# Optimization experiments

Hardware: AMD Instinct MI355X
Metric: run time of the kernel (lower is better)

## Reference

```python
import jax, jax.numpy as jnp
import numpy as np

N_NODES = 25000
N_EDGES = 250000
F_IN = 32
F_OUT = 32
EDGE_DIM = 6
H1, H2 = 64, 128


def setup_inputs() -> dict:
    key = jax.random.key(0)
    ks = jax.random.split(key, 10)
    s = 0.05
    return {
        "x": jax.random.normal(ks[0], (N_NODES, F_IN), dtype=jnp.float32),
        "edge_attr": jax.random.normal(ks[1], (N_EDGES, EDGE_DIM), dtype=jnp.float32),
        # fnet MLP params: Linear(6->64), ReLU, Linear(64->128), ReLU, Linear(128->F_IN*F_OUT)
        "W1": jax.random.normal(ks[2], (H1, EDGE_DIM), dtype=jnp.float32) * s,
        "b1": jnp.zeros((H1,), dtype=jnp.float32),
        "W2": jax.random.normal(ks[3], (H2, H1), dtype=jnp.float32) * s,
        "b2": jnp.zeros((H2,), dtype=jnp.float32),
        "W3": jax.random.normal(ks[4], (F_IN * F_OUT, H2), dtype=jnp.float32) * s,
        "b3": jnp.zeros((F_IN * F_OUT,), dtype=jnp.float32),
        "edge_src": jax.random.randint(ks[5], (N_EDGES,), 0, N_NODES),
        "edge_dst": jax.random.randint(ks[6], (N_EDGES,), 0, N_NODES),
    }


def reference(x, edge_attr, W1, b1, W2, b2, W3, b3, edge_src, edge_dst):
    # fnet: per-edge MLP producing a dynamic filter theta_e of shape [F_OUT, F_IN]
    h = jax.nn.relu(edge_attr @ W1.T + b1)            # [E, H1]
    h = jax.nn.relu(h @ W2.T + b2)                    # [E, H2]
    theta = (h @ W3.T + b3).reshape(-1, F_OUT, F_IN)  # [E, F_OUT, F_IN]
    # gather source features, apply per-edge filter
    msg = jnp.einsum('eoi,ei->eo', theta, x[edge_src])  # [E, F_OUT]
    # scatter-mean over destination nodes (ECC averages over neighborhood)
    agg = jax.ops.segment_sum(msg, edge_dst, num_segments=N_NODES)
    deg = jax.ops.segment_sum(jnp.ones((msg.shape[0],), x.dtype), edge_dst,
                              num_segments=N_NODES)
    out = agg / jnp.maximum(deg, 1.0)[:, None]        # [N, F_OUT]
    return jax.nn.relu(out)                           # trailing 'r' in config
```

## Files before the change

### kernel.cpp

```cpp
#include <hip/hip_runtime.h>
#include <hip/hip_fp16.h>

#define N_NODES 25000
#define N_EDGES 250000
#define ED 6
#define H1 64
#define H2 128
#define NBLK 977
#define NCHUNK 33
#define CHUNK_USH 4096
#define W3S_USHORTS (NCHUNK*CHUNK_USH)
#define W2S_USHORTS (H2*H1)
#define SCAN_BLOCKS 98

typedef float f32x4 __attribute__((ext_vector_type(4)));
typedef float f32x16 __attribute__((ext_vector_type(16)));
typedef _Float16 f16x8 __attribute__((ext_vector_type(8)));
typedef __fp16 fp16x2 __attribute__((ext_vector_type(2)));
typedef unsigned int u32x4 __attribute__((ext_vector_type(4)));
typedef unsigned int u32x2 __attribute__((ext_vector_type(2)));

union F16x8U { u32x4 u; f16x8 h; };
union PKU    { fp16x2 p; unsigned u; };

__device__ __forceinline__ unsigned pkrtz(float lo, float hi) {
    PKU r; r.p = __builtin_amdgcn_cvt_pkrtz(lo, hi); return r.u;
}
__device__ __forceinline__ unsigned pk_mul_blo(unsigned h, unsigned x) {
    unsigned d;
    asm("v_pk_mul_f16 %0, %1, %2 op_sel:[0,0] op_sel_hi:[0,1]" : "=v"(d) : "v"(h), "v"(x));
    return d;
}
__device__ __forceinline__ unsigned pk_mul_bhi(unsigned h, unsigned x) {
    unsigned d;
    asm("v_pk_mul_f16 %0, %1, %2 op_sel:[1,0] op_sel_hi:[1,1]" : "=v"(d) : "v"(h), "v"(x));
    return d;
}
__device__ __forceinline__ f32x4 mfma16(f16x8 a, f16x8 b, f32x4 c) {
    return __builtin_amdgcn_mfma_f32_16x16x32_f16(a, b, c, 0, 0, 0);
}
__device__ __forceinline__ f32x16 mfma32(f16x8 a, f16x8 b, f32x16 c) {
    return __builtin_amdgcn_mfma_f32_32x32x16_f16(a, b, c, 0, 0, 0);
}
__device__ __forceinline__ void gload16(const void* g, void* l) {
    __builtin_amdgcn_global_load_lds(
        (const __attribute__((address_space(1))) unsigned int*)g,
        (__attribute__((address_space(3))) unsigned int*)l, 16, 0, 0);
}

__global__ __launch_bounds__(256) void ecc_init(
    const float* __restrict__ W3, const float* __restrict__ b3,
    const float* __restrict__ W2,
    unsigned* __restrict__ cnt, unsigned short* __restrict__ w3s,
    unsigned short* __restrict__ w2s, float* __restrict__ agg)
{
    int idx = blockIdx.x * 256 + threadIdx.x;
    if (idx < W3S_USHORTS) {
        int c = idx >> 12, r = idx & 4095;
        int ks = r >> 9;
        int lane = (r >> 3) & 63;
        int j = r & 7;
        int o = lane & 31;
        int kp = c * 128 + ks * 16 + ((lane >> 5) << 3) + j;
        float v = 0.f;
        if (kp < 4096)      { int k = kp >> 5, i = kp & 31; v = W3[(o * 32 + i) * 128 + k]; }
        else if (kp < 4128) { v = b3[o * 32 + (kp - 4096)]; }
        __half hv = __float2half_rn(v);
        w3s[idx] = *reinterpret_cast<unsigned short*>(&hv);
    }
    if (idx < W2S_USHORTS) {
        __half hv = __float2half_rn(W2[idx]);
        w2s[idx] = *reinterpret_cast<unsigned short*>(&hv);
    }
    if (idx < N_NODES) cnt[idx] = 0u;
    if (idx < N_NODES * 32) agg[idx] = 0.f;
}

__global__ __launch_bounds__(256) void ecc_hist(
    const int* __restrict__ dst, unsigned* __restrict__ cnt,
    unsigned* __restrict__ rank)
{
    int e = blockIdx.x * 256 + threadIdx.x;
    if (e < N_EDGES) rank[e] = atomicAdd(&cnt[dst[e]], 1u);
}

__global__ __launch_bounds__(256) void ecc_scan1(
    const unsigned* __restrict__ cnt, unsigned* __restrict__ off,
    unsigned* __restrict__ bsum)
{
    __shared__ unsigned s[256];
    const int t = threadIdx.x, i = blockIdx.x * 256 + t;
    unsigned v = (i < N_NODES) ? cnt[i] : 0u;
    s[t] = v; __syncthreads();
    #pragma unroll
    for (int d = 1; d < 256; d <<= 1) {
        unsigned add = (t >= d) ? s[t - d] : 0u;
        __syncthreads(); s[t] += add; __syncthreads();
    }
    if (i < N_NODES) off[i] = s[t] - v;
    if (t == 255) bsum[blockIdx.x] = s[255];
}

__global__ __launch_bounds__(256) void ecc_scan23(
    unsigned* __restrict__ off, const unsigned* __restrict__ bsum)
{
    __shared__ unsigned sbase;
    const int t = threadIdx.x, b = blockIdx.x;
    if (t < 64) {
        unsigned v = 0u;
        if (t < b) v = bsum[t];
        if (t + 64 < b) v += bsum[t + 64];
        #pragma unroll
        for (int d = 32; d >= 1; d >>= 1) v += __shfl_down(v, d, 64);
        if (t == 0) sbase = v;
    }
    __syncthreads();
    const int i = b * 256 + t;
    if (i < N_NODES) off[i] += sbase;
    if (b == 0 && t == 0) off[N_NODES] = N_EDGES;
}

__global__ __launch_bounds__(256) void ecc_perm(
    const int* __restrict__ dst, const unsigned* __restrict__ off,
    const unsigned* __restrict__ rank, unsigned* __restrict__ perm,
    int* __restrict__ bfirst)
{
    int e = blockIdx.x * 256 + threadIdx.x;
    if (e < N_EDGES) perm[off[dst[e]] + rank[e]] = (unsigned)e;
    if (e < NBLK) {
        const unsigned tile = (unsigned)e * 256u;
        int loN = 0, hiN = N_NODES;
        while (loN < hiN) {
            int mid = (loN + hiN) >> 1;
            if (off[mid + 1] > tile) hiN = mid; else loN = mid + 1;
        }
        bfirst[e] = loN;
    }
}

__global__ __launch_bounds__(256) void ecc_fused(
    const float* __restrict__ x,   const float* __restrict__ ea,
    const float* __restrict__ W1,  const float* __restrict__ b1,
    const unsigned short* __restrict__ w2s, const float* __restrict__ b2,
    const unsigned short* __restrict__ w3s,
    const int* __restrict__ src,   const unsigned* __restrict__ perm,
    const unsigned* __restrict__ off, const int* __restrict__ bfirst,
    float* __restrict__ agg)
{
    __shared__ __align__(16) unsigned short sm[256 * H2];
    __shared__ __align__(16) unsigned short wbuf[2][CHUNK_USH];

    const int t = threadIdx.x;
    const int tile = blockIdx.x * 256;
    const int slot = tile + t;
    const bool ev = (slot < N_EDGES);
    const unsigned je = ev ? perm[slot] : 0u;

    const int w = t >> 6, l = t & 63, lr = l & 15, kg = l >> 4;
    const int l31 = l & 31, l5 = l >> 5;

    gload16(w3s + t * 8,        &wbuf[0][t * 8]);
    gload16(w3s + 2048 + t * 8, &wbuf[0][2048 + t * 8]);

    {
        float a[ED];
        #pragma unroll
        for (int c = 0; c < ED; ++c) a[c] = ev ? ea[(long)je * ED + c] : 0.f;

        float h1[H1];
        #pragma unroll
        for (int o = 0; o < H1; ++o) {
            float acc = b1[o];
            #pragma unroll
            for (int c = 0; c < ED; ++c) acc = fmaf(W1[o * ED + c], a[c], acc);
            h1[o] = fmaxf(acc, 0.f);
        }
        #pragma unroll
        for (int q = 0; q < 8; ++q) {
            u32x4 pk;
            #pragma unroll
            for (int j = 0; j < 4; ++j)
                pk[j] = pkrtz(h1[q*8 + 2*j], h1[q*8 + 2*j + 1]);
            const int boff = (t * 128 + q * 16) ^ ((t & 7) << 4);
            *(u32x4*)((char*)sm + boff) = pk;
        }
    }

    unsigned xsh[2][8];
    #pragma unroll
    for (int mt = 0; mt < 2; ++mt) {
        const int er = tile + w * 64 + mt * 32 + l31;
        if (er < N_EDGES) {
            const float* xb = x + (long)src[perm[er]] * 32;
            const float4* xp = (const float4*)(xb + l5 * 8);
            const float4* xq = (const float4*)(xb + 16 + l5 * 8);
            float4 v0 = xp[0], v1 = xp[1], v2 = xq[0], v3 = xq[1];
            xsh[mt][0] = pkrtz(v0.x, v0.y); xsh[mt][1] = pkrtz(v0.z, v0.w);
            xsh[mt][2] = pkrtz(v1.x, v1.y); xsh[mt][3] = pkrtz(v1.z, v1.w);
            xsh[mt][4] = pkrtz(v2.x, v2.y); xsh[mt][5] = pkrtz(v2.z, v2.w);
            xsh[mt][6] = pkrtz(v3.x, v3.y); xsh[mt][7] = pkrtz(v3.z, v3.w);
        } else {
            #pragma unroll
            for (int j = 0; j < 8; ++j) xsh[mt][j] = 0u;
        }
    }

    {
        F16x8U hb[4][2];
        #pragma unroll
        for (int ne = 0; ne < 4; ++ne) {
            const int er = w * 64 + ne * 16 + lr;
            #pragma unroll
            for (int ks = 0; ks < 2; ++ks) {
                const int boff = (er * 128 + ks * 64 + kg * 16) ^ ((er & 7) << 4);
                hb[ne][ks].u = *(const u32x4*)((const char*)sm + boff);
            }
        }
        __syncthreads();

        #pragma unroll
        for (int mo = 0; mo < 8; ++mo) {
            F16x8U a2[2];
            #pragma unroll
            for (int ks = 0; ks < 2; ++ks)
                a2[ks].u = *(const u32x4*)(w2s + (mo*16 + lr) * 64 + ks*32 + kg*8);
            const float4 bv = *(const float4*)(b2 + mo*16 + kg*4);
            #pragma unroll
            for (int ne = 0; ne < 4; ++ne) {
                f32x4 c = (f32x4){0.f, 0.f, 0.f, 0.f};
                c = mfma16(a2[0].h, hb[ne][0].h, c);
                c = mfma16(a2[1].h, hb[ne][1].h, c);
                const unsigned p0 = pkrtz(fmaxf(c[0]+bv.x, 0.f), fmaxf(c[1]+bv.y, 0.f));
                const unsigned p1 = pkrtz(fmaxf(c[2]+bv.z, 0.f), fmaxf(c[3]+bv.w, 0.f));
                const int er = w * 64 + ne * 16 + lr;
                const int boff = (er * 256 + (mo*16 + kg*4) * 2) ^ ((er & 7) << 4);
                *(u32x2*)((char*)sm + boff) = (u32x2){p0, p1};
            }
        }
    }

    f32x16 acc[2];
    #pragma unroll
    for (int i = 0; i < 16; ++i) { acc[0][i] = 0.f; acc[1][i] = 0.f; }

    __syncthreads();

    int cur = 0;
    #pragma unroll 1
    for (int c = 0; c < 32; ++c) {
        {
            const unsigned short* gs = w3s + (c + 1) * CHUNK_USH + t * 8;
            gload16(gs,        &wbuf[cur ^ 1][t * 8]);
            gload16(gs + 2048, &wbuf[cur ^ 1][2048 + t * 8]);
        }
        const char* wb = (const char*)wbuf[cur] + l * 16;

        u32x2 hv[2];
        #pragma unroll
        for (int mt = 0; mt < 2; ++mt) {
            const int row = w * 64 + mt * 32 + l31;
            const int boff = (row * 256 + c * 8) ^ ((row & 7) << 4);
            hv[mt] = *(const u32x2*)((const char*)sm + boff);
        }

        #pragma unroll
        for (int ks = 0; ks < 8; ++ks) {
            F16x8U bf;
            bf.u = *(const u32x4*)(wb + ks * 1024);
            const int kl = ks >> 1;
            const int xb = (ks & 1) * 4;
            #pragma unroll
            for (int mt = 0; mt < 2; ++mt) {
                const unsigned h01 = hv[mt][kl >> 1];
                F16x8U af;
                if (kl & 1) {
                    af.u[0] = pk_mul_bhi(h01, xsh[mt][xb + 0]);
                    af.u[1] = pk_mul_bhi(h01, xsh[mt][xb + 1]);
                    af.u[2] = pk_mul_bhi(h01, xsh[mt][xb + 2]);
                    af.u[3] = pk_mul_bhi(h01, xsh[mt][xb + 3]);
                } else {
                    af.u[0] = pk_mul_blo(h01, xsh[mt][xb + 0]);
                    af.u[1] = pk_mul_blo(h01, xsh[mt][xb + 1]);
                    af.u[2] = pk_mul_blo(h01, xsh[mt][xb + 2]);
                    af.u[3] = pk_mul_blo(h01, xsh[mt][xb + 3]);
                }
                acc[mt] = mfma32(af.h, bf.h, acc[mt]);
            }
        }

        __syncthreads();
        cur ^= 1;
    }
    {
        const char* wb = (const char*)wbuf[cur] + l * 16;
        F16x8U bf0, bf1;
        bf0.u = *(const u32x4*)(wb);
        bf1.u = *(const u32x4*)(wb + 1024);
        #pragma unroll
        for (int mt = 0; mt < 2; ++mt) {
            F16x8U af;
            af.u = (u32x4){xsh[mt][0], xsh[mt][1], xsh[mt][2], xsh[mt][3]};
            acc[mt] = mfma32(af.h, bf0.h, acc[mt]);
            af.u = (u32x4){xsh[mt][4], xsh[mt][5], xsh[mt][6], xsh[mt][7]};
            acc[mt] = mfma32(af.h, bf1.h, acc[mt]);
        }
    }

    __syncthreads();
    {
        unsigned short* msgl = (unsigned short*)sm;
        #pragma unroll
        for (int mt = 0; mt < 2; ++mt) {
            #pragma unroll
            for (int rg = 0; rg < 16; ++rg) {
                const int el = w * 64 + mt * 32 + (rg & 3) + 8 * (rg >> 2) + 4 * l5;
                PKU hv2; hv2.p = __builtin_amdgcn_cvt_pkrtz(acc[mt][rg], 0.f);
                msgl[el * 32 + l31] = (unsigned short)(hv2.u & 0xFFFFu);
            }
        }
    }
    __syncthreads();

    {
        const unsigned short* msgl = (const unsigned short*)sm;
        const int n0 = bfirst[blockIdx.x];
        const int tend = tile + 256;
        #pragma unroll 1
        for (int p = t; ; p += 256) {
            const int n = n0 + (p >> 5);
            if (n >= N_NODES) break;
            const unsigned lo = off[n], hi = off[n + 1];
            if ((int)lo >= tend) break;
            const int o = p & 31;
            const int jb = max((int)lo, tile), jend = min((int)hi, tend);
            if (jend > jb) {
                float s = 0.f;
                for (int j = jb; j < jend; ++j) {
                    union { unsigned short u; _Float16 h; } v;
                    v.u = msgl[(j - tile) * 32 + o];
                    s += (float)v.h;
                }
                atomicAdd(&agg[(long)n * 32 + o], s);
            }
        }
    }
}

__global__ __launch_bounds__(256) void ecc_finalize(
    const float* __restrict__ agg, const unsigned* __restrict__ cnt,
    float* __restrict__ out)
{
    const int i = blockIdx.x * 256 + threadIdx.x;
    if (i >= N_NODES * 32) return;
    const int n = i >> 5;
    const float d = fmaxf((float)cnt[n], 1.f);
    out[i] = fmaxf(agg[i] / d, 0.f);
}

extern "C" void kernel_launch(void* const* d_in, const int* in_sizes, int n_in,
                              void* d_out, int out_size, void* d_ws, size_t ws_size,
                              hipStream_t stream) {
    const float* x   = (const float*)d_in[0];
    const float* ea  = (const float*)d_in[1];
    const float* W1  = (const float*)d_in[2];
    const float* b1  = (const float*)d_in[3];
    const float* W2  = (const float*)d_in[4];
    const float* b2  = (const float*)d_in[5];
    const float* W3  = (const float*)d_in[6];
    const float* b3  = (const float*)d_in[7];
    const int*   src = (const int*)d_in[8];
    const int*   dst = (const int*)d_in[9];
    float* out = (float*)d_out;

    char* p = (char*)d_ws;
    unsigned short* w3s = (unsigned short*)p; p += W3S_USHORTS * 2;
    unsigned short* w2s = (unsigned short*)p; p += 16384;
    unsigned* cnt   = (unsigned*)p; p += 100096;
    unsigned* off   = (unsigned*)p; p += 100352;
    unsigned* bsum  = (unsigned*)p; p += 512;
    int*      bfirst= (int*)p;      p += 4096;
    unsigned* rank  = (unsigned*)p; p += 1000192;
    unsigned* perm  = (unsigned*)p; p += 1000192;
    float*    agg   = (float*)p;

    ecc_init<<<(N_NODES * 32 + 255) / 256, 256, 0, stream>>>(W3, b3, W2, cnt, w3s, w2s, agg);
    ecc_hist<<<NBLK, 256, 0, stream>>>(dst, cnt, rank);
    ecc_scan1<<<SCAN_BLOCKS, 256, 0, stream>>>(cnt, off, bsum);
    ecc_scan23<<<SCAN_BLOCKS, 256, 0, stream>>>(off, bsum);
    ecc_perm<<<NBLK, 256, 0, stream>>>(dst, off, rank, perm, bfirst);
    ecc_fused<<<NBLK, 256, 0, stream>>>(x, ea, W1, b1, w2s, b2, w3s, src, perm, off, bfirst, agg);
    ecc_finalize<<<(N_NODES * 32 + 255) / 256, 256, 0, stream>>>(agg, cnt, out);
}
```

Before: 125.0 us.

## Halve edges per block to 128 and split layer-1 work across thread halves

The fused kernel now processes 128 edges per 256-thread block instead of 256, launching twice as many blocks. Each wave handles one 32-row MFMA tile rather than two, and the two thread halves split the 64 hidden units of layer 1. This halves accumulator and register state and shared memory per block, aiming for higher occupancy and better load balance, at the cost of streaming W3 chunks from global memory twice as often per edge. It also raises wave priority around the MFMA loop and stores messages in shared memory as fp32 instead of fp16, which avoids the conversions and keeps full precision before the atomic adds.

```diff
diff --git a/kernel.cpp b/kernel.cpp
--- a/kernel.cpp
+++ b/kernel.cpp
@@ -7,6 +7,8 @@
 #define H1 64
 #define H2 128
 #define NBLK 977
+#define EPB 128
+#define NBLK2 1954
 #define NCHUNK 33
 #define CHUNK_USH 4096
 #define W3S_USHORTS (NCHUNK*CHUNK_USH)
@@ -127,8 +129,8 @@
 {
     int e = blockIdx.x * 256 + threadIdx.x;
     if (e < N_EDGES) perm[off[dst[e]] + rank[e]] = (unsigned)e;
-    if (e < NBLK) {
-        const unsigned tile = (unsigned)e * 256u;
+    if (e < NBLK2) {
+        const unsigned tile = (unsigned)e * EPB;
         int loN = 0, hiN = N_NODES;
         while (loN < hiN) {
             int mid = (loN + hiN) >> 1;
@@ -147,69 +149,72 @@
     const unsigned* __restrict__ off, const int* __restrict__ bfirst,
     float* __restrict__ agg)
 {
-    __shared__ __align__(16) unsigned short sm[256 * H2];
+    __shared__ __align__(16) unsigned short sm[EPB * H2];
     __shared__ __align__(16) unsigned short wbuf[2][CHUNK_USH];
 
     const int t = threadIdx.x;
-    const int tile = blockIdx.x * 256;
-    const int slot = tile + t;
-    const bool ev = (slot < N_EDGES);
-    const unsigned je = ev ? perm[slot] : 0u;
+    const int tile = blockIdx.x * EPB;
 
     const int w = t >> 6, l = t & 63, lr = l & 15, kg = l >> 4;
     const int l31 = l & 31, l5 = l >> 5;
+    const int e_loc = t & 127, half = t >> 7;
 
     gload16(w3s + t * 8,        &wbuf[0][t * 8]);
     gload16(w3s + 2048 + t * 8, &wbuf[0][2048 + t * 8]);
 
     {
+        const int slot = tile + e_loc;
+        const bool ev = (slot < N_EDGES);
+        const unsigned je = ev ? perm[slot] : 0u;
         float a[ED];
         #pragma unroll
         for (int c = 0; c < ED; ++c) a[c] = ev ? ea[(long)je * ED + c] : 0.f;
 
-        float h1[H1];
-        #pragma unroll
-        for (int o = 0; o < H1; ++o) {
+        float h1[32];
+        #pragma unroll
+        for (int o2 = 0; o2 < 32; ++o2) {
+            const int o = half * 32 + o2;
             float acc = b1[o];
             #pragma unroll
             for (int c = 0; c < ED; ++c) acc = fmaf(W1[o * ED + c], a[c], acc);
-            h1[o] = fmaxf(acc, 0.f);
-        }
-        #pragma unroll
-        for (int q = 0; q < 8; ++q) {
+            h1[o2] = fmaxf(acc, 0.f);
+        }
+        #pragma unroll
+        for (int q = 0; q < 4; ++q) {
             u32x4 pk;
             #pragma unroll
             for (int j = 0; j < 4; ++j)
                 pk[j] = pkrtz(h1[q*8 + 2*j], h1[q*8 + 2*j + 1]);
-            const int boff = (t * 128 + q * 16) ^ ((t & 7) << 4);
+            const int boff = (e_loc * 128 + half * 64 + q * 16) ^ ((e_loc & 7) << 4);
             *(u32x4*)((char*)sm + boff) = pk;
         }
     }
 
-    unsigned xsh[2][8];
-    #pragma unroll
-    for (int mt = 0; mt < 2; ++mt) {
-        const int er = tile + w * 64 + mt * 32 + l31;
+    __syncthreads();
+
+    unsigned xsh[8];
+    {
+        const int er = tile + w * 32 + l31;
         if (er < N_EDGES) {
             const float* xb = x + (long)src[perm[er]] * 32;
             const float4* xp = (const float4*)(xb + l5 * 8);
             const float4* xq = (const float4*)(xb + 16 + l5 * 8);
             float4 v0 = xp[0], v1 = xp[1], v2 = xq[0], v3 = xq[1];
-            xsh[mt][0] = pkrtz(v0.x, v0.y); xsh[mt][1] = pkrtz(v0.z, v0.w);
-            xsh[mt][2] = pkrtz(v1.x, v1.y); xsh[mt][3] = pkrtz(v1.z, v1.w);
-            xsh[mt][4] = pkrtz(v2.x, v2.y); xsh[mt][5] = pkrtz(v2.z, v2.w);
-            xsh[mt][6] = pkrtz(v3.x, v3.y); xsh[mt][7] = pkrtz(v3.z, v3.w);
+            xsh[0] = pkrtz(v0.x, v0.y); xsh[1] = pkrtz(v0.z, v0.w);
+            xsh[2] = pkrtz(v1.x, v1.y); xsh[3] = pkrtz(v1.z, v1.w);
+            xsh[4] = pkrtz(v2.x, v2.y); xsh[5] = pkrtz(v2.z, v2.w);
+            xsh[6] = pkrtz(v3.x, v3.y); xsh[7] = pkrtz(v3.z, v3.w);
         } else {
             #pragma unroll
-            for (int j = 0; j < 8; ++j) xsh[mt][j] = 0u;
-        }
-    }
-
-    {
-        F16x8U hb[4][2];
-        #pragma unroll
-        for (int ne = 0; ne < 4; ++ne) {
-            const int er = w * 64 + ne * 16 + lr;
+            for (int j = 0; j < 8; ++j) xsh[j] = 0u;
+        }
+    }
+
+    {
+        F16x8U hb[2][2];
+        #pragma unroll
+        for (int ne = 0; ne < 2; ++ne) {
+            const int er = (w * 2 + ne) * 16 + lr;
             #pragma unroll
             for (int ks = 0; ks < 2; ++ks) {
                 const int boff = (er * 128 + ks * 64 + kg * 16) ^ ((er & 7) << 4);
@@ -226,23 +231,24 @@
                 a2[ks].u = *(const u32x4*)(w2s + (mo*16 + lr) * 64 + ks*32 + kg*8);
             const float4 bv = *(const float4*)(b2 + mo*16 + kg*4);
             #pragma unroll
-            for (int ne = 0; ne < 4; ++ne) {
+            for (int ne = 0; ne < 2; ++ne) {
                 f32x4 c = (f32x4){0.f, 0.f, 0.f, 0.f};
                 c = mfma16(a2[0].h, hb[ne][0].h, c);
                 c = mfma16(a2[1].h, hb[ne][1].h, c);
                 const unsigned p0 = pkrtz(fmaxf(c[0]+bv.x, 0.f), fmaxf(c[1]+bv.y, 0.f));
                 const unsigned p1 = pkrtz(fmaxf(c[2]+bv.z, 0.f), fmaxf(c[3]+bv.w, 0.f));
-                const int er = w * 64 + ne * 16 + lr;
+                const int er = (w * 2 + ne) * 16 + lr;
                 const int boff = (er * 256 + (mo*16 + kg*4) * 2) ^ ((er & 7) << 4);
                 *(u32x2*)((char*)sm + boff) = (u32x2){p0, p1};
             }
         }
     }
 
-    f32x16 acc[2];
+    f32x16 acc;
     #pragma unroll
-    for (int i = 0; i < 16; ++i) { acc[0][i] = 0.f; acc[1][i] = 0.f; }
-
+    for (int i = 0; i < 16; ++i) acc[i] = 0.f;
+
+    const int row = w * 32 + l31;
     __syncthreads();
 
     int cur = 0;
@@ -255,38 +261,32 @@
         }
         const char* wb = (const char*)wbuf[cur] + l * 16;
 
-        u32x2 hv[2];
-        #pragma unroll
-        for (int mt = 0; mt < 2; ++mt) {
-            const int row = w * 64 + mt * 32 + l31;
-            const int boff = (row * 256 + c * 8) ^ ((row & 7) << 4);
-            hv[mt] = *(const u32x2*)((const char*)sm + boff);
-        }
-
+        const int boff = (row * 256 + c * 8) ^ ((row & 7) << 4);
+        const u32x2 hv = *(const u32x2*)((const char*)sm + boff);
+
+        __builtin_amdgcn_s_setprio(1);
         #pragma unroll
         for (int ks = 0; ks < 8; ++ks) {
             F16x8U bf;
             bf.u = *(const u32x4*)(wb + ks * 1024);
             const int kl = ks >> 1;
             const int xb = (ks & 1) * 4;
-            #pragma unroll
-            for (int mt = 0; mt < 2; ++mt) {
-                const unsigned h01 = hv[mt][kl >> 1];
-                F16x8U af;
-                if (kl & 1) {
-                    af.u[0] = pk_mul_bhi(h01, xsh[mt][xb + 0]);
-                    af.u[1] = pk_mul_bhi(h01, xsh[mt][xb + 1]);
-                    af.u[2] = pk_mul_bhi(h01, xsh[mt][xb + 2]);
-                    af.u[3] = pk_mul_bhi(h01, xsh[mt][xb + 3]);
-                } else {
-                    af.u[0] = pk_mul_blo(h01, xsh[mt][xb + 0]);
-                    af.u[1] = pk_mul_blo(h01, xsh[mt][xb + 1]);
-                    af.u[2] = pk_mul_blo(h01, xsh[mt][xb + 2]);
-                    af.u[3] = pk_mul_blo(h01, xsh[mt][xb + 3]);
-                }
-                acc[mt] = mfma32(af.h, bf.h, acc[mt]);
+            const unsigned h01 = hv[kl >> 1];
+            F16x8U af;
+            if (kl & 1) {
+                af.u[0] = pk_mul_bhi(h01, xsh[xb + 0]);
+                af.u[1] = pk_mul_bhi(h01, xsh[xb + 1]);
+                af.u[2] = pk_mul_bhi(h01, xsh[xb + 2]);
+                af.u[3] = pk_mul_bhi(h01, xsh[xb + 3]);
+            } else {
+                af.u[0] = pk_mul_blo(h01, xsh[xb + 0]);
+                af.u[1] = pk_mul_blo(h01, xsh[xb + 1]);
+                af.u[2] = pk_mul_blo(h01, xsh[xb + 2]);
+                af.u[3] = pk_mul_blo(h01, xsh[xb + 3]);
             }
-        }
+            acc = mfma32(af.h, bf.h, acc);
+        }
+        __builtin_amdgcn_s_setprio(0);
 
         __syncthreads();
         cur ^= 1;
@@ -296,35 +296,28 @@
         F16x8U bf0, bf1;
         bf0.u = *(const u32x4*)(wb);
         bf1.u = *(const u32x4*)(wb + 1024);
-        #pragma unroll
-        for (int mt = 0; mt < 2; ++mt) {
-            F16x8U af;
-            af.u = (u32x4){xsh[mt][0], xsh[mt][1], xsh[mt][2], xsh[mt][3]};
-            acc[mt] = mfma32(af.h, bf0.h, acc[mt]);
-            af.u = (u32x4){xsh[mt][4], xsh[mt][5], xsh[mt][6], xsh[mt][7]};
-            acc[mt] = mfma32(af.h, bf1.h, acc[mt]);
-        }
-    }
-
-    __syncthreads();
-    {
-        unsigned short* msgl = (unsigned short*)sm;
-        #pragma unroll
-        for (int mt = 0; mt < 2; ++mt) {
-            #pragma unroll
-            for (int rg = 0; rg < 16; ++rg) {
-                const int el = w * 64 + mt * 32 + (rg & 3) + 8 * (rg >> 2) + 4 * l5;
-                PKU hv2; hv2.p = __builtin_amdgcn_cvt_pkrtz(acc[mt][rg], 0.f);
-                msgl[el * 32 + l31] = (unsigned short)(hv2.u & 0xFFFFu);
-            }
-        }
-    }
-    __syncthreads();
-
-    {
-        const unsigned short* msgl = (const unsigned short*)sm;
+        F16x8U af;
+        af.u = (u32x4){xsh[0], xsh[1], xsh[2], xsh[3]};
+        acc = mfma32(af.h, bf0.h, acc);
+        af.u = (u32x4){xsh[4], xsh[5], xsh[6], xsh[7]};
+        acc = mfma32(af.h, bf1.h, acc);
+    }
+
+    __syncthreads();
+    {
+        float* pm = (float*)sm;
+        #pragma unroll
+        for (int rg = 0; rg < 16; ++rg) {
+            const int el = w * 32 + (rg & 3) + 8 * (rg >> 2) + 4 * l5;
+            pm[el * 32 + l31] = acc[rg];
+        }
+    }
+    __syncthreads();
+
+    {
+        const float* pm = (const float*)sm;
         const int n0 = bfirst[blockIdx.x];
-        const int tend = tile + 256;
+        const int tend = tile + EPB;
         #pragma unroll 1
         for (int p = t; ; p += 256) {
             const int n = n0 + (p >> 5);
@@ -335,11 +328,7 @@
             const int jb = max((int)lo, tile), jend = min((int)hi, tend);
             if (jend > jb) {
                 float s = 0.f;
-                for (int j = jb; j < jend; ++j) {
-                    union { unsigned short u; _Float16 h; } v;
-                    v.u = msgl[(j - tile) * 32 + o];
-                    s += (float)v.h;
-                }
+                for (int j = jb; j < jend; ++j) s += pm[(j - tile) * 32 + o];
                 atomicAdd(&agg[(long)n * 32 + o], s);
             }
         }
@@ -378,7 +367,7 @@
     unsigned* cnt   = (unsigned*)p; p += 100096;
     unsigned* off   = (unsigned*)p; p += 100352;
     unsigned* bsum  = (unsigned*)p; p += 512;
-    int*      bfirst= (int*)p;      p += 4096;
+    int*      bfirst= (int*)p;      p += 8192;
     unsigned* rank  = (unsigned*)p; p += 1000192;
     unsigned* perm  = (unsigned*)p; p += 1000192;
     float*    agg   = (float*)p;
@@ -388,6 +377,6 @@
     ecc_scan1<<<SCAN_BLOCKS, 256, 0, stream>>>(cnt, off, bsum);
     ecc_scan23<<<SCAN_BLOCKS, 256, 0, stream>>>(off, bsum);
     ecc_perm<<<NBLK, 256, 0, stream>>>(dst, off, rank, perm, bfirst);
-    ecc_fused<<<NBLK, 256, 0, stream>>>(x, ea, W1, b1, w2s, b2, w3s, src, perm, off, bfirst, agg);
+    ecc_fused<<<NBLK2, 256, 0, stream>>>(x, ea, W1, b1, w2s, b2, w3s, src, perm, off, bfirst, agg);
     ecc_finalize<<<(N_NODES * 32 + 255) / 256, 256, 0, stream>>>(agg, cnt, out);
 }
```

Result: slower. 141.6 us (+13.3%).

## Deepen W3 LDS pipeline to 4 half-size buffers with prefetch distance two

Applied to the files above, without the earlier changes.

Splits the W3 weight stream into 66 chunks of 2048 halves and cycles them through four LDS buffers, issuing each load two iterations ahead. A partial vmcnt wait plus a raw s_barrier replaces the full __syncthreads per iteration. MFMA sections are wrapped in s_setprio so compute waves get priority. This is meant to hide global-to-LDS load latency behind MFMA work, at the cost of twice as many loop iterations and barriers and more reliance on exact waitcnt accounting.

```diff
diff --git a/kernel.cpp b/kernel.cpp
--- a/kernel.cpp
+++ b/kernel.cpp
@@ -7,8 +7,8 @@
 #define H1 64
 #define H2 128
 #define NBLK 977
-#define NCHUNK 33
-#define CHUNK_USH 4096
+#define NCHUNK 66
+#define CHUNK_USH 2048
 #define W3S_USHORTS (NCHUNK*CHUNK_USH)
 #define W2S_USHORTS (H2*H1)
 #define SCAN_BLOCKS 98
@@ -56,12 +56,12 @@
 {
     int idx = blockIdx.x * 256 + threadIdx.x;
     if (idx < W3S_USHORTS) {
-        int c = idx >> 12, r = idx & 4095;
+        int c = idx >> 11, r = idx & 2047;
         int ks = r >> 9;
         int lane = (r >> 3) & 63;
         int j = r & 7;
         int o = lane & 31;
-        int kp = c * 128 + ks * 16 + ((lane >> 5) << 3) + j;
+        int kp = c * 64 + ks * 16 + ((lane >> 5) << 3) + j;
         float v = 0.f;
         if (kp < 4096)      { int k = kp >> 5, i = kp & 31; v = W3[(o * 32 + i) * 128 + k]; }
         else if (kp < 4128) { v = b3[o * 32 + (kp - 4096)]; }
@@ -148,7 +148,7 @@
     float* __restrict__ agg)
 {
     __shared__ __align__(16) unsigned short sm[256 * H2];
-    __shared__ __align__(16) unsigned short wbuf[2][CHUNK_USH];
+    __shared__ __align__(16) unsigned short wbuf[4][CHUNK_USH];
 
     const int t = threadIdx.x;
     const int tile = blockIdx.x * 256;
@@ -159,8 +159,8 @@
     const int w = t >> 6, l = t & 63, lr = l & 15, kg = l >> 4;
     const int l31 = l & 31, l5 = l >> 5;
 
-    gload16(w3s + t * 8,        &wbuf[0][t * 8]);
-    gload16(w3s + 2048 + t * 8, &wbuf[0][2048 + t * 8]);
+    gload16(w3s + t * 8,             &wbuf[0][t * 8]);
+    gload16(w3s + CHUNK_USH + t * 8, &wbuf[1][t * 8]);
 
     {
         float a[ED];
@@ -245,54 +245,62 @@
 
     __syncthreads();
 
-    int cur = 0;
+#define COMPUTE(cc) do {                                                    \
+        const char* wb = (const char*)wbuf + ((cc) & 3) * 4096 + l * 16;    \
+        unsigned hv[2];                                                     \
+        _Pragma("unroll")                                                   \
+        for (int mt = 0; mt < 2; ++mt) {                                    \
+            const int row = w * 64 + mt * 32 + l31;                         \
+            const int boff = (row * 256 + (cc) * 4) ^ ((row & 7) << 4);     \
+            hv[mt] = *(const unsigned*)((const char*)sm + boff);            \
+        }                                                                   \
+        __builtin_amdgcn_s_setprio(1);                                      \
+        _Pragma("unroll")                                                   \
+        for (int ks = 0; ks < 4; ++ks) {                                    \
+            F16x8U bf;                                                      \
+            bf.u = *(const u32x4*)(wb + ks * 1024);                         \
+            const int kl = ks >> 1;                                         \
+            const int xb = (ks & 1) * 4;                                    \
+            _Pragma("unroll")                                               \
+            for (int mt = 0; mt < 2; ++mt) {                                \
+                F16x8U af;                                                  \
+                if (kl & 1) {                                               \
+                    af.u[0] = pk_mul_bhi(hv[mt], xsh[mt][xb + 0]);          \
+                    af.u[1] = pk_mul_bhi(hv[mt], xsh[mt][xb + 1]);          \
+                    af.u[2] = pk_mul_bhi(hv[mt], xsh[mt][xb + 2]);          \
+                    af.u[3] = pk_mul_bhi(hv[mt], xsh[mt][xb + 3]);          \
+                } else {                                                    \
+                    af.u[0] = pk_mul_blo(hv[mt], xsh[mt][xb + 0]);          \
+                    af.u[1] = pk_mul_blo(hv[mt], xsh[mt][xb + 1]);          \
+                    af.u[2] = pk_mul_blo(hv[mt], xsh[mt][xb + 2]);          \
+                    af.u[3] = pk_mul_blo(hv[mt], xsh[mt][xb + 3]);          \
+                }                                                           \
+                acc[mt] = mfma32(af.h, bf.h, acc[mt]);                      \
+            }                                                               \
+        }                                                                   \
+        __builtin_amdgcn_s_setprio(0);                                      \
+    } while (0)
+
     #pragma unroll 1
-    for (int c = 0; c < 32; ++c) {
-        {
-            const unsigned short* gs = w3s + (c + 1) * CHUNK_USH + t * 8;
-            gload16(gs,        &wbuf[cur ^ 1][t * 8]);
-            gload16(gs + 2048, &wbuf[cur ^ 1][2048 + t * 8]);
-        }
-        const char* wb = (const char*)wbuf[cur] + l * 16;
-
-        u32x2 hv[2];
-        #pragma unroll
-        for (int mt = 0; mt < 2; ++mt) {
-            const int row = w * 64 + mt * 32 + l31;
-            const int boff = (row * 256 + c * 8) ^ ((row & 7) << 4);
-            hv[mt] = *(const u32x2*)((const char*)sm + boff);
-        }
-
-        #pragma unroll
-        for (int ks = 0; ks < 8; ++ks) {
-            F16x8U bf;
-            bf.u = *(const u32x4*)(wb + ks * 1024);
-            const int kl = ks >> 1;
-            const int xb = (ks & 1) * 4;
-            #pragma unroll
-            for (int mt = 0; mt < 2; ++mt) {
-                const unsigned h01 = hv[mt][kl >> 1];
-                F16x8U af;
-                if (kl & 1) {
-                    af.u[0] = pk_mul_bhi(h01, xsh[mt][xb + 0]);
-                    af.u[1] = pk_mul_bhi(h01, xsh[mt][xb + 1]);
-                    af.u[2] = pk_mul_bhi(h01, xsh[mt][xb + 2]);
-                    af.u[3] = pk_mul_bhi(h01, xsh[mt][xb + 3]);
-                } else {
-                    af.u[0] = pk_mul_blo(h01, xsh[mt][xb + 0]);
-                    af.u[1] = pk_mul_blo(h01, xsh[mt][xb + 1]);
-                    af.u[2] = pk_mul_blo(h01, xsh[mt][xb + 2]);
-                    af.u[3] = pk_mul_blo(h01, xsh[mt][xb + 3]);
-                }
-                acc[mt] = mfma32(af.h, bf.h, acc[mt]);
-            }
-        }
-
-        __syncthreads();
-        cur ^= 1;
-    }
-    {
-        const char* wb = (const char*)wbuf[cur] + l * 16;
+    for (int c = 0; c < 63; ++c) {
+        const unsigned short* gs = w3s + (c + 2) * CHUNK_USH + t * 8;
+        gload16(gs, &wbuf[(c + 2) & 3][t * 8]);
+        asm volatile("s_waitcnt vmcnt(2)" ::: "memory");
+        __builtin_amdgcn_s_barrier();
+        __builtin_amdgcn_sched_barrier(0);
+        COMPUTE(c);
+    }
+    {
+        asm volatile("s_waitcnt vmcnt(1)" ::: "memory");
+        __builtin_amdgcn_s_barrier();
+        __builtin_amdgcn_sched_barrier(0);
+        COMPUTE(63);
+    }
+    {
+        asm volatile("s_waitcnt vmcnt(0)" ::: "memory");
+        __builtin_amdgcn_s_barrier();
+        __builtin_amdgcn_sched_barrier(0);
+        const char* wb = (const char*)wbuf + (64 & 3) * 4096 + l * 16;
         F16x8U bf0, bf1;
         bf0.u = *(const u32x4*)(wb);
         bf1.u = *(const u32x4*)(wb + 1024);
@@ -305,6 +313,7 @@
             acc[mt] = mfma32(af.h, bf1.h, acc[mt]);
         }
     }
+#undef COMPUTE
 
     __syncthreads();
     {
```

Measured after the change: 130.9 us. +4.8%, slower.
